# Optimization experiments

Hardware: AMD Instinct MI355X
Metric: run time of the kernel (lower is better)

## Reference

```python
import jax, jax.numpy as jnp
import numpy as np

DIM = 768
HEADS = 12
N_PATCH = 1024
ORDER = 5
DECAY = 0.5
EPS = 1e-6


def _exact_mask(N, order, decay):
    # 2D grid graph adjacency, row-major node order (matches sorted nx.grid_2d_graph nodes)
    side = int(np.sqrt(N))
    A = np.zeros((N, N), dtype=np.float64)
    idx = np.arange(N)
    r, c = idx // side, idx % side
    right = idx[c < side - 1]
    A[right, right + 1] = 1.0
    A[right + 1, right] = 1.0
    down = idx[r < side - 1]
    A[down, down + side] = 1.0
    A[down + side, down] = 1.0
    D_inv = 1.0 / np.maximum(A.sum(axis=1), 1.0)
    W = D_inv[:, None] * A
    M = np.eye(N)
    W_k = np.eye(N)
    coeff = 1.0
    for _ in range(order):
        W_k = W_k @ W
        coeff *= decay
        M += coeff * W_k
    M = M / M.sum(axis=1, keepdims=True)
    return jnp.asarray(M, dtype=jnp.float32)


def setup_inputs() -> dict:
    key = jax.random.key(0)
    k1, k2, k3, k4 = jax.random.split(key, 4)
    B = 4
    x = jax.random.normal(k1, (B, N_PATCH, DIM), dtype=jnp.float32)
    # nn.Linear(dim, 3*dim, bias=False): store as [dim, 3*dim] for x @ W
    scale = 1.0 / np.sqrt(DIM)
    W_qkv = jax.random.uniform(k2, (DIM, 3 * DIM), dtype=jnp.float32, minval=-scale, maxval=scale)
    W_out = jax.random.uniform(k3, (DIM, DIM), dtype=jnp.float32, minval=-scale, maxval=scale)
    b_out = jax.random.uniform(k4, (DIM,), dtype=jnp.float32, minval=-scale, maxval=scale)
    mask = _exact_mask(N_PATCH, ORDER, DECAY)
    return {"x": x, "W_qkv": W_qkv, "W_out": W_out, "b_out": b_out, "mask": mask}


def reference(x, W_qkv, W_out, b_out, mask):
    B, N, C = x.shape
    H, D = HEADS, C // HEADS
    qkv = x @ W_qkv  # [B, N, 3C]
    q, k, v = jnp.split(qkv, 3, axis=-1)
    # [B, N, C] -> [B, H, N, D]
    q, k, v = (t.reshape(B, N, H, D).transpose(0, 2, 1, 3) for t in (q, k, v))
    # feature map
    q = jax.nn.relu(q) + EPS
    k = jax.nn.relu(k) + EPS
    # (q^T @ M)^T = M^T @ q  ->  einsum over node axis
    q_graph = jnp.einsum('nm,bhnd->bhmd', mask, q)
    k_graph = jnp.einsum('nm,bhnd->bhmd', mask, k)
    q = q + 0.1 * q_graph
    k = k + 0.1 * k_graph
    linear_kernel = jnp.einsum('bhnd,bhmd->bhnm', q, k)  # [B, H, N, N]
    masked_kernel = linear_kernel * mask[None, None, :, :]
    z = 1.0 / (masked_kernel.sum(axis=-1, keepdims=True) + EPS)  # [B, H, N, 1]
    out = jnp.einsum('bhnm,bhmd->bhnd', masked_kernel, v) * z
    out = out.transpose(0, 2, 1, 3).reshape(B, N, C)
    return out @ W_out + b_out
```

## Files before the change

### kernel.cpp

```cpp
#include <hip/hip_runtime.h>

#define NP   1024
#define DIM  768
#define NH   12
#define HD   64
#define TQ   2304
#define EPS  1e-6f

typedef __attribute__((ext_vector_type(8))) short bf16x8;
typedef __attribute__((ext_vector_type(4))) float f32x4;

#define MFMA(a, b, c) __builtin_amdgcn_mfma_f32_16x16x32_bf16((a), (b), (c), 0, 0, 0)

__device__ __forceinline__ unsigned short f2b(float x) {
    unsigned int u = __builtin_bit_cast(unsigned int, x);
    u = (u + 0x7fffu + ((u >> 16) & 1u)) >> 16;
    return (unsigned short)u;
}
__device__ __forceinline__ float b2f(unsigned short h) {
    unsigned int u = ((unsigned int)h) << 16;
    return __builtin_bit_cast(float, u);
}
#if __has_builtin(__builtin_amdgcn_cvt_pk_bf16_f32)
typedef __attribute__((ext_vector_type(2))) __bf16 bf16x2t;
__device__ __forceinline__ unsigned int pk2(float lo, float hi) {
    bf16x2t v = __builtin_amdgcn_cvt_pk_bf16_f32(lo, hi);
    return __builtin_bit_cast(unsigned int, v);
}
#else
__device__ __forceinline__ unsigned int pk2(float lo, float hi) {
    return (unsigned int)f2b(lo) | ((unsigned int)f2b(hi) << 16);
}
#endif
__device__ __forceinline__ void gld16(const void* g, void* l) {
    __builtin_amdgcn_global_load_lds((const __attribute__((address_space(1))) unsigned int*)g,
                                     (__attribute__((address_space(3))) unsigned int*)l,
                                     16, 0, 0);
}

__global__ __launch_bounds__(256) void k_prep(const float* __restrict__ x,
                                              const float* __restrict__ W_qkv,
                                              const float* __restrict__ W_out,
                                              const float* __restrict__ mask,
                                              unsigned short* __restrict__ xb,
                                              unsigned short* __restrict__ WqkvT,
                                              unsigned short* __restrict__ WoutT,
                                              unsigned short* __restrict__ M2) {
    __shared__ float buf[64][65];
    const int bx = blockIdx.x, t = threadIdx.x;
    if (bx < 1536) {
        const int i = bx * 256 + t;
        const float4* p = (const float4*)x + (size_t)i * 2;
        float4 a = p[0], b = p[1];
        alignas(16) unsigned short o[8] = {f2b(a.x), f2b(a.y), f2b(a.z), f2b(a.w),
                                           f2b(b.x), f2b(b.y), f2b(b.z), f2b(b.w)};
        *(uint4*)(xb + (size_t)i * 8) = *(const uint4*)o;
        return;
    }
    const float* in; unsigned short* outp; int R, C, ct, rt; bool isMask = false;
    if (bx < 1968)      { int q = bx - 1536; in = W_qkv; outp = WqkvT; R = 768;  C = 2304; ct = q % 36; rt = q / 36; }
    else if (bx < 2112) { int q = bx - 1968; in = W_out; outp = WoutT; R = 768;  C = 768;  ct = q % 12; rt = q / 12; }
    else                { int q = bx - 2112; in = mask;  outp = M2;    R = 1024; C = 1024; ct = q % 16; rt = q / 16; isMask = true; }
    const int r0 = rt * 64, c0 = ct * 64;
    const int rr = t >> 4, cc = (t & 15) * 4;
    #pragma unroll
    for (int p = 0; p < 4; ++p) {
        float4 v = *(const float4*)(in + (size_t)(r0 + p * 16 + rr) * C + c0 + cc);
        buf[p * 16 + rr][cc + 0] = v.x; buf[p * 16 + rr][cc + 1] = v.y;
        buf[p * 16 + rr][cc + 2] = v.z; buf[p * 16 + rr][cc + 3] = v.w;
    }
    __syncthreads();
    const int oc = t >> 2, orr = (t & 3) * 16;
    alignas(16) unsigned short tmp[16];
    if (isMask) {
        #pragma unroll
        for (int j = 0; j < 16; ++j) {
            float v = 0.1f * buf[orr + j][oc] + ((c0 + oc) == (r0 + orr + j) ? 1.f : 0.f);
            tmp[j] = f2b(v);
        }
    } else {
        #pragma unroll
        for (int j = 0; j < 16; ++j) tmp[j] = f2b(buf[orr + j][oc]);
    }
    unsigned short* dst = outp + (size_t)(c0 + oc) * R + r0 + orr;
    *(uint4*)dst = *(const uint4*)tmp;
    *(uint4*)(dst + 8) = *(const uint4*)(tmp + 8);
}

__global__ __launch_bounds__(512) void k_gemm1(const unsigned short* __restrict__ A,
                                               const unsigned short* __restrict__ Bt,
                                               unsigned short* __restrict__ T) {
    __shared__ unsigned short As[128][32];
    __shared__ unsigned short Bs[128][32];
    const int tid = threadIdx.x, w = tid >> 6, l = tid & 63;
    const int bid = blockIdx.x;
    const int mstrip = (bid & 7) * 4 + ((bid >> 3) & 3);
    const int nstrip = bid >> 5;
    const int m0 = mstrip * 128, n0 = nstrip * 128;
    const int wm = (w & 3) * 32, wn = (w >> 2) * 64;
    const int quad = l >> 4, col = l & 15;
    const int lr = l >> 2, lc = (l & 3) * 8;

    f32x4 acc[2][4] = {};
    for (int k0 = 0; k0 < DIM; k0 += 32) {
        gld16(A + (size_t)(m0 + w * 16 + lr) * DIM + k0 + lc, &As[w * 16][0]);
        gld16(Bt + (size_t)(n0 + w * 16 + lr) * DIM + k0 + lc, &Bs[w * 16][0]);
        __syncthreads();
        bf16x8 a[2], b[4];
        #pragma unroll
        for (int i = 0; i < 2; ++i) a[i] = *(const bf16x8*)&As[wm + i * 16 + col][quad * 8];
        #pragma unroll
        for (int j = 0; j < 4; ++j) b[j] = *(const bf16x8*)&Bs[wn + j * 16 + col][quad * 8];
        #pragma unroll
        for (int i = 0; i < 2; ++i)
            #pragma unroll
            for (int j = 0; j < 4; ++j)
                acc[i][j] = MFMA(a[i], b[j], acc[i][j]);
        __syncthreads();
    }

    const int cgb = n0 + wn;
    const int slot = cgb / DIM;
    const int h = (cgb % DIM) >> 6;
    const bool act = (slot < 2);
    const int sh = slot * 48 + (m0 >> 10) * NH + h;
    const int npb = (m0 & 1023) + wm + quad * 4;
    #pragma unroll
    for (int j = 0; j < 4; ++j) {
        unsigned short* dcol = T + ((size_t)(sh * HD + j * 16 + col)) * NP + npb;
        #pragma unroll
        for (int i = 0; i < 2; ++i) {
            float v0 = acc[i][j][0], v1 = acc[i][j][1], v2 = acc[i][j][2], v3 = acc[i][j][3];
            if (act) {
                v0 = fmaxf(v0, 0.f) + EPS; v1 = fmaxf(v1, 0.f) + EPS;
                v2 = fmaxf(v2, 0.f) + EPS; v3 = fmaxf(v3, 0.f) + EPS;
            }
            uint2 o; o.x = pk2(v0, v1); o.y = pk2(v2, v3);
            *(uint2*)(dcol + i * 16) = o;
        }
    }
}

__global__ __launch_bounds__(256) void k_graphmix(const unsigned short* __restrict__ M2,
                                                  const unsigned short* __restrict__ T,
                                                  unsigned short* __restrict__ q2) {
    const int bh = blockIdx.y, mt = blockIdx.x;
    const int m0 = mt * 64;
    __shared__ unsigned short M2s[2][64][32], Fq[2][64][32], Fk[2][64][32];
    const int tid = threadIdx.x, w = tid >> 6, l = tid & 63;
    const int quad = l >> 4, col = l & 15;
    const int lr = l >> 2, lc = (l & 3) * 8;
    const unsigned short* Tq = T + (size_t)bh * HD * NP;
    const unsigned short* Tk = T + (size_t)(48 + bh) * HD * NP;

    f32x4 accq[4] = {}, acck[4] = {};
    const int c0 = max(0, mt - 3), c1 = min(15, mt + 3);
    for (int c = c0; c <= c1; ++c) {
        const int nc = c * 64;
        __syncthreads();
        #pragma unroll
        for (int hh = 0; hh < 2; ++hh) {
            gld16(M2 + (size_t)(m0 + w * 16 + lr) * NP + nc + hh * 32 + lc, &M2s[hh][w * 16][0]);
            gld16(Tq + (size_t)(w * 16 + lr) * NP + nc + hh * 32 + lc, &Fq[hh][w * 16][0]);
            gld16(Tk + (size_t)(w * 16 + lr) * NP + nc + hh * 32 + lc, &Fk[hh][w * 16][0]);
        }
        __syncthreads();
        #pragma unroll
        for (int ks = 0; ks < 2; ++ks) {
            bf16x8 bm = *(const bf16x8*)&M2s[ks][w * 16 + col][quad * 8];
            #pragma unroll
            for (int dt = 0; dt < 4; ++dt) {
                bf16x8 aq = *(const bf16x8*)&Fq[ks][dt * 16 + col][quad * 8];
                bf16x8 ak = *(const bf16x8*)&Fk[ks][dt * 16 + col][quad * 8];
                accq[dt] = MFMA(aq, bm, accq[dt]);
                acck[dt] = MFMA(ak, bm, acck[dt]);
            }
        }
    }
    unsigned short* q2q = q2 + ((size_t)bh * NP + m0 + w * 16 + col) * HD;
    unsigned short* q2k = q2 + ((size_t)(48 + bh) * NP + m0 + w * 16 + col) * HD;
    #pragma unroll
    for (int dt = 0; dt < 4; ++dt) {
        const int d0 = dt * 16 + quad * 4;
        uint2 oq; oq.x = pk2(accq[dt][0], accq[dt][1]); oq.y = pk2(accq[dt][2], accq[dt][3]);
        uint2 ok; ok.x = pk2(acck[dt][0], acck[dt][1]); ok.y = pk2(acck[dt][2], acck[dt][3]);
        *(uint2*)(q2q + d0) = oq;
        *(uint2*)(q2k + d0) = ok;
    }
}

__global__ __launch_bounds__(256) void k_attn(const unsigned short* __restrict__ q2,
                                              const unsigned short* __restrict__ T,
                                              const float* __restrict__ mask,
                                              unsigned short* __restrict__ attnb) {
    const int bh = blockIdx.y, b = bh / NH, h = bh % NH;
    const int nt = blockIdx.x, n0 = nt * 64;
    __shared__ unsigned short Qs[2][64][32];
    __shared__ unsigned short Ks[2][64][32];
    __shared__ unsigned short VT[2][64][32];
    __shared__ unsigned int Ss2[32][68];
    __shared__ float rowz[64];
    const int tid = threadIdx.x, w = tid >> 6, l = tid & 63;
    const int quad = l >> 4, col = l & 15;
    const int lr = l >> 2, lc = (l & 3) * 8;

    const unsigned short* qb = q2 + ((size_t)bh * NP + n0) * HD;
    const unsigned short* kb = q2 + (size_t)(48 + bh) * NP * HD;
    const unsigned short* vtb = T + (size_t)(96 + bh) * HD * NP;

    #pragma unroll
    for (int hh = 0; hh < 2; ++hh)
        gld16(qb + (size_t)(w * 16 + lr) * HD + hh * 32 + lc, &Qs[hh][w * 16][0]);

    f32x4 oacc[4] = {};
    float racc[4] = {};
    const int mlo = max(0, nt - 3), mhi = min(15, nt + 3);
    const unsigned int sel = (col & 1) ? 0x07060302u : 0x05040100u;

    for (int mt = mlo; mt <= mhi; ++mt) {
        const int m0 = mt * 64;
        __syncthreads();
        #pragma unroll
        for (int hh = 0; hh < 2; ++hh) {
            gld16(kb + (size_t)(m0 + w * 16 + lr) * HD + hh * 32 + lc, &Ks[hh][w * 16][0]);
            gld16(vtb + (size_t)(w * 16 + lr) * NP + m0 + hh * 32 + lc, &VT[hh][w * 16][0]);
        }
        float mreg[4][4];
        #pragma unroll
        for (int mtt = 0; mtt < 4; ++mtt)
            #pragma unroll
            for (int r = 0; r < 4; ++r)
                mreg[mtt][r] = mask[(size_t)(n0 + w * 16 + quad * 4 + r) * NP
                                    + m0 + mtt * 16 + col];
        __syncthreads();

        f32x4 s[4] = {};
        #pragma unroll
        for (int ks = 0; ks < 2; ++ks) {
            bf16x8 aq = *(const bf16x8*)&Qs[ks][w * 16 + col][quad * 8];
            #pragma unroll
            for (int mtt = 0; mtt < 4; ++mtt) {
                bf16x8 bk = *(const bf16x8*)&Ks[ks][mtt * 16 + col][quad * 8];
                s[mtt] = MFMA(aq, bk, s[mtt]);
            }
        }
        {
            const int npr = w * 8 + quad * 2;
            #pragma unroll
            for (int mtt = 0; mtt < 4; ++mtt) {
                float v0 = s[mtt][0] * mreg[mtt][0];
                float v1 = s[mtt][1] * mreg[mtt][1];
                float v2 = s[mtt][2] * mreg[mtt][2];
                float v3 = s[mtt][3] * mreg[mtt][3];
                racc[0] += v0; racc[1] += v1; racc[2] += v2; racc[3] += v3;
                Ss2[npr][mtt * 16 + col]     = pk2(v0, v1);
                Ss2[npr + 1][mtt * 16 + col] = pk2(v2, v3);
            }
        }
        __syncthreads();
        #pragma unroll
        for (int ks = 0; ks < 2; ++ks) {
            const unsigned int* rp = &Ss2[w * 8 + (col >> 1)][ks * 32 + quad * 8];
            uint4 U  = *(const uint4*)rp;
            uint4 U2 = *(const uint4*)(rp + 4);
            uint4 fr;
            fr.x = __builtin_amdgcn_perm(U.y,  U.x,  sel);
            fr.y = __builtin_amdgcn_perm(U.w,  U.z,  sel);
            fr.z = __builtin_amdgcn_perm(U2.y, U2.x, sel);
            fr.w = __builtin_amdgcn_perm(U2.w, U2.z, sel);
            bf16x8 as = __builtin_bit_cast(bf16x8, fr);
            #pragma unroll
            for (int dt = 0; dt < 4; ++dt) {
                bf16x8 bv = *(const bf16x8*)&VT[ks][dt * 16 + col][quad * 8];
                oacc[dt] = MFMA(as, bv, oacc[dt]);
            }
        }
    }

    #pragma unroll
    for (int r = 0; r < 4; ++r) {
        float v = racc[r];
        v += __shfl_xor(v, 1); v += __shfl_xor(v, 2);
        v += __shfl_xor(v, 4); v += __shfl_xor(v, 8);
        if (col == 0) rowz[w * 16 + quad * 4 + r] = v;
    }
    __syncthreads();
    #pragma unroll
    for (int r = 0; r < 4; ++r) {
        const int nl = w * 16 + quad * 4 + r;
        const float z = 1.f / (rowz[nl] + EPS);
        #pragma unroll
        for (int dt = 0; dt < 4; ++dt)
            attnb[(size_t)(b * NP + n0 + nl) * DIM + h * HD + dt * 16 + col] =
                f2b(oacc[dt][r] * z);
    }
}

__global__ __launch_bounds__(256) void k_gemm2(const unsigned short* __restrict__ A,
                                               const unsigned short* __restrict__ Bt,
                                               const float* __restrict__ bias,
                                               float* __restrict__ C) {
    __shared__ unsigned short As[128][32];
    __shared__ unsigned short Bs[64][32];
    const int tid = threadIdx.x, w = tid >> 6, l = tid & 63;
    const int bid = blockIdx.x;
    const int mstrip = (bid & 7) * 4 + ((bid >> 3) & 3);
    const int nstrip = bid >> 5;
    const int m0 = mstrip * 128, n0 = nstrip * 64;
    const int wm = (w >> 1) * 64, wn = (w & 1) * 32;
    const int quad = l >> 4, col = l & 15;
    const int lr = l >> 2, lc = (l & 3) * 8;

    f32x4 acc[4][2] = {};
    for (int k0 = 0; k0 < DIM; k0 += 32) {
        gld16(A + (size_t)(m0 + w * 32 + lr) * DIM + k0 + lc, &As[w * 32][0]);
        gld16(A + (size_t)(m0 + w * 32 + 16 + lr) * DIM + k0 + lc, &As[w * 32 + 16][0]);
        gld16(Bt + (size_t)(n0 + w * 16 + lr) * DIM + k0 + lc, &Bs[w * 16][0]);
        __syncthreads();
        bf16x8 a[4], b[2];
        #pragma unroll
        for (int i = 0; i < 4; ++i) a[i] = *(const bf16x8*)&As[wm + i * 16 + col][quad * 8];
        #pragma unroll
        for (int j = 0; j < 2; ++j) b[j] = *(const bf16x8*)&Bs[wn + j * 16 + col][quad * 8];
        #pragma unroll
        for (int i = 0; i < 4; ++i)
            #pragma unroll
            for (int j = 0; j < 2; ++j)
                acc[i][j] = MFMA(a[i], b[j], acc[i][j]);
        __syncthreads();
    }
    #pragma unroll
    for (int i = 0; i < 4; ++i)
        #pragma unroll
        for (int j = 0; j < 2; ++j) {
            const int n = n0 + wn + j * 16 + col;
            #pragma unroll
            for (int r = 0; r < 4; ++r) {
                const int m = m0 + wm + i * 16 + quad * 4 + r;
                C[(size_t)m * DIM + n] = acc[i][j][r] + bias[n];
            }
        }
}

extern "C" void kernel_launch(void* const* d_in, const int* in_sizes, int n_in,
                              void* d_out, int out_size, void* d_ws, size_t ws_size,
                              hipStream_t stream) {
    (void)in_sizes; (void)n_in; (void)out_size; (void)ws_size;
    const float* x     = (const float*)d_in[0];
    const float* W_qkv = (const float*)d_in[1];
    const float* W_out = (const float*)d_in[2];
    const float* b_out = (const float*)d_in[3];
    const float* mask  = (const float*)d_in[4];
    float* out = (float*)d_out;

    unsigned short* p = (unsigned short*)d_ws;
    unsigned short* xb    = p; p += (size_t)4096 * DIM;
    unsigned short* WqkvT = p; p += (size_t)TQ * DIM;
    unsigned short* WoutT = p; p += (size_t)DIM * DIM;
    unsigned short* M2    = p; p += (size_t)NP * NP;
    unsigned short* T     = p; p += (size_t)3 * 48 * HD * NP;
    unsigned short* q2    = p; p += (size_t)2 * 48 * NP * HD;
    unsigned short* attnb = p; p += (size_t)4096 * DIM;

    k_prep<<<dim3(2368), 256, 0, stream>>>(x, W_qkv, W_out, mask, xb, WqkvT, WoutT, M2);
    k_gemm1<<<dim3(576), 512, 0, stream>>>(xb, WqkvT, T);
    k_graphmix<<<dim3(NP / 64, 48), 256, 0, stream>>>(M2, T, q2);
    k_attn<<<dim3(NP / 64, 48), 256, 0, stream>>>(q2, T, mask, attnb);
    k_gemm2<<<dim3(384), 256, 0, stream>>>(attnb, WoutT, b_out, out);
}
```

Before: 163.0 us.

## Fuse x bf16 conversion into QKV GEMM, tighten band windows, retile output GEMM

The separate x-to-bf16 pass in the prep kernel is removed; the QKV GEMM now reads fp32 x directly and converts it while staging into LDS, which saves a full write and re-read of the activation. The QKV and output GEMMs now process 64-wide K steps (two 32-wide halves per sync), halving barrier count. The graph-mix and attention band loops switch from seven 64-wide tiles to a 32-aligned window of 384 columns, trimming work outside the mask band. The output GEMM uses 64x64 tiles with twice as many blocks to improve occupancy, at the cost of more redundant operand loads.

New measurement: 156.8 us. 3.8% less time.

```diff
diff --git a/kernel.cpp b/kernel.cpp
--- a/kernel.cpp
+++ b/kernel.cpp
@@ -38,29 +38,18 @@
                                      16, 0, 0);
 }
 
-__global__ __launch_bounds__(256) void k_prep(const float* __restrict__ x,
-                                              const float* __restrict__ W_qkv,
+__global__ __launch_bounds__(256) void k_prep(const float* __restrict__ W_qkv,
                                               const float* __restrict__ W_out,
                                               const float* __restrict__ mask,
-                                              unsigned short* __restrict__ xb,
                                               unsigned short* __restrict__ WqkvT,
                                               unsigned short* __restrict__ WoutT,
                                               unsigned short* __restrict__ M2) {
     __shared__ float buf[64][65];
     const int bx = blockIdx.x, t = threadIdx.x;
-    if (bx < 1536) {
-        const int i = bx * 256 + t;
-        const float4* p = (const float4*)x + (size_t)i * 2;
-        float4 a = p[0], b = p[1];
-        alignas(16) unsigned short o[8] = {f2b(a.x), f2b(a.y), f2b(a.z), f2b(a.w),
-                                           f2b(b.x), f2b(b.y), f2b(b.z), f2b(b.w)};
-        *(uint4*)(xb + (size_t)i * 8) = *(const uint4*)o;
-        return;
-    }
     const float* in; unsigned short* outp; int R, C, ct, rt; bool isMask = false;
-    if (bx < 1968)      { int q = bx - 1536; in = W_qkv; outp = WqkvT; R = 768;  C = 2304; ct = q % 36; rt = q / 36; }
-    else if (bx < 2112) { int q = bx - 1968; in = W_out; outp = WoutT; R = 768;  C = 768;  ct = q % 12; rt = q / 12; }
-    else                { int q = bx - 2112; in = mask;  outp = M2;    R = 1024; C = 1024; ct = q % 16; rt = q / 16; isMask = true; }
+    if (bx < 432)      { int q = bx;       in = W_qkv; outp = WqkvT; R = 768;  C = 2304; ct = q % 36; rt = q / 36; }
+    else if (bx < 576) { int q = bx - 432; in = W_out; outp = WoutT; R = 768;  C = 768;  ct = q % 12; rt = q / 12; }
+    else               { int q = bx - 576; in = mask;  outp = M2;    R = 1024; C = 1024; ct = q % 16; rt = q / 16; isMask = true; }
     const int r0 = rt * 64, c0 = ct * 64;
     const int rr = t >> 4, cc = (t & 15) * 4;
     #pragma unroll
@@ -87,11 +76,11 @@
     *(uint4*)(dst + 8) = *(const uint4*)(tmp + 8);
 }
 
-__global__ __launch_bounds__(512) void k_gemm1(const unsigned short* __restrict__ A,
+__global__ __launch_bounds__(512) void k_gemm1(const float* __restrict__ X,
                                                const unsigned short* __restrict__ Bt,
                                                unsigned short* __restrict__ T) {
-    __shared__ unsigned short As[128][32];
-    __shared__ unsigned short Bs[128][32];
+    __shared__ unsigned short As[2][128][32];
+    __shared__ unsigned short Bs[2][128][32];
     const int tid = threadIdx.x, w = tid >> 6, l = tid & 63;
     const int bid = blockIdx.x;
     const int mstrip = (bid & 7) * 4 + ((bid >> 3) & 3);
@@ -100,22 +89,35 @@
     const int wm = (w & 3) * 32, wn = (w >> 2) * 64;
     const int quad = l >> 4, col = l & 15;
     const int lr = l >> 2, lc = (l & 3) * 8;
+    const int arow = tid >> 2, akc = (tid & 3) * 8;
 
     f32x4 acc[2][4] = {};
-    for (int k0 = 0; k0 < DIM; k0 += 32) {
-        gld16(A + (size_t)(m0 + w * 16 + lr) * DIM + k0 + lc, &As[w * 16][0]);
-        gld16(Bt + (size_t)(n0 + w * 16 + lr) * DIM + k0 + lc, &Bs[w * 16][0]);
-        __syncthreads();
-        bf16x8 a[2], b[4];
-        #pragma unroll
-        for (int i = 0; i < 2; ++i) a[i] = *(const bf16x8*)&As[wm + i * 16 + col][quad * 8];
-        #pragma unroll
-        for (int j = 0; j < 4; ++j) b[j] = *(const bf16x8*)&Bs[wn + j * 16 + col][quad * 8];
-        #pragma unroll
-        for (int i = 0; i < 2; ++i)
-            #pragma unroll
-            for (int j = 0; j < 4; ++j)
-                acc[i][j] = MFMA(a[i], b[j], acc[i][j]);
+    for (int k0 = 0; k0 < DIM; k0 += 64) {
+        #pragma unroll
+        for (int hh = 0; hh < 2; ++hh) {
+            gld16(Bt + (size_t)(n0 + w * 16 + lr) * DIM + k0 + hh * 32 + lc, &Bs[hh][w * 16][0]);
+            const float* xp = X + (size_t)(m0 + arow) * DIM + k0 + hh * 32 + akc;
+            float4 xa = *(const float4*)xp;
+            float4 xb = *(const float4*)(xp + 4);
+            uint4 o;
+            o.x = pk2(xa.x, xa.y); o.y = pk2(xa.z, xa.w);
+            o.z = pk2(xb.x, xb.y); o.w = pk2(xb.z, xb.w);
+            *(uint4*)&As[hh][arow][akc] = o;
+        }
+        __syncthreads();
+        #pragma unroll
+        for (int hh = 0; hh < 2; ++hh) {
+            bf16x8 a[2], b[4];
+            #pragma unroll
+            for (int i = 0; i < 2; ++i) a[i] = *(const bf16x8*)&As[hh][wm + i * 16 + col][quad * 8];
+            #pragma unroll
+            for (int j = 0; j < 4; ++j) b[j] = *(const bf16x8*)&Bs[hh][wn + j * 16 + col][quad * 8];
+            #pragma unroll
+            for (int i = 0; i < 2; ++i)
+                #pragma unroll
+                for (int j = 0; j < 4; ++j)
+                    acc[i][j] = MFMA(a[i], b[j], acc[i][j]);
+        }
         __syncthreads();
     }
 
@@ -146,7 +148,7 @@
                                                   unsigned short* __restrict__ q2) {
     const int bh = blockIdx.y, mt = blockIdx.x;
     const int m0 = mt * 64;
-    __shared__ unsigned short M2s[2][64][32], Fq[2][64][32], Fk[2][64][32];
+    __shared__ unsigned short M2s[4][64][32], Fq[4][64][32], Fk[4][64][32];
     const int tid = threadIdx.x, w = tid >> 6, l = tid & 63;
     const int quad = l >> 4, col = l & 15;
     const int lr = l >> 2, lc = (l & 3) * 8;
@@ -154,19 +156,19 @@
     const unsigned short* Tk = T + (size_t)(48 + bh) * HD * NP;
 
     f32x4 accq[4] = {}, acck[4] = {};
-    const int c0 = max(0, mt - 3), c1 = min(15, mt + 3);
-    for (int c = c0; c <= c1; ++c) {
-        const int nc = c * 64;
-        __syncthreads();
-        #pragma unroll
-        for (int hh = 0; hh < 2; ++hh) {
+    const int nr0 = min(max(2 * mt - 5, 0), 20) * 32;
+    for (int it = 0; it < 3; ++it) {
+        const int nc = nr0 + it * 128;
+        __syncthreads();
+        #pragma unroll
+        for (int hh = 0; hh < 4; ++hh) {
             gld16(M2 + (size_t)(m0 + w * 16 + lr) * NP + nc + hh * 32 + lc, &M2s[hh][w * 16][0]);
             gld16(Tq + (size_t)(w * 16 + lr) * NP + nc + hh * 32 + lc, &Fq[hh][w * 16][0]);
             gld16(Tk + (size_t)(w * 16 + lr) * NP + nc + hh * 32 + lc, &Fk[hh][w * 16][0]);
         }
         __syncthreads();
         #pragma unroll
-        for (int ks = 0; ks < 2; ++ks) {
+        for (int ks = 0; ks < 4; ++ks) {
             bf16x8 bm = *(const bf16x8*)&M2s[ks][w * 16 + col][quad * 8];
             #pragma unroll
             for (int dt = 0; dt < 4; ++dt) {
@@ -214,11 +216,11 @@
 
     f32x4 oacc[4] = {};
     float racc[4] = {};
-    const int mlo = max(0, nt - 3), mhi = min(15, nt + 3);
+    const int mr0 = min(max(2 * nt - 5, 0), 20) * 32;
     const unsigned int sel = (col & 1) ? 0x07060302u : 0x05040100u;
 
-    for (int mt = mlo; mt <= mhi; ++mt) {
-        const int m0 = mt * 64;
+    for (int it = 0; it < 6; ++it) {
+        const int m0 = mr0 + it * 64;
         __syncthreads();
         #pragma unroll
         for (int hh = 0; hh < 2; ++hh) {
@@ -300,37 +302,42 @@
                                                const unsigned short* __restrict__ Bt,
                                                const float* __restrict__ bias,
                                                float* __restrict__ C) {
-    __shared__ unsigned short As[128][32];
-    __shared__ unsigned short Bs[64][32];
+    __shared__ unsigned short As[2][64][32];
+    __shared__ unsigned short Bs[2][64][32];
     const int tid = threadIdx.x, w = tid >> 6, l = tid & 63;
     const int bid = blockIdx.x;
-    const int mstrip = (bid & 7) * 4 + ((bid >> 3) & 3);
-    const int nstrip = bid >> 5;
-    const int m0 = mstrip * 128, n0 = nstrip * 64;
-    const int wm = (w >> 1) * 64, wn = (w & 1) * 32;
+    const int mstrip = (bid & 7) * 8 + ((bid >> 3) & 7);
+    const int nstrip = bid >> 6;
+    const int m0 = mstrip * 64, n0 = nstrip * 64;
+    const int wm = (w & 1) * 32, wn = (w >> 1) * 32;
     const int quad = l >> 4, col = l & 15;
     const int lr = l >> 2, lc = (l & 3) * 8;
 
-    f32x4 acc[4][2] = {};
-    for (int k0 = 0; k0 < DIM; k0 += 32) {
-        gld16(A + (size_t)(m0 + w * 32 + lr) * DIM + k0 + lc, &As[w * 32][0]);
-        gld16(A + (size_t)(m0 + w * 32 + 16 + lr) * DIM + k0 + lc, &As[w * 32 + 16][0]);
-        gld16(Bt + (size_t)(n0 + w * 16 + lr) * DIM + k0 + lc, &Bs[w * 16][0]);
-        __syncthreads();
-        bf16x8 a[4], b[2];
-        #pragma unroll
-        for (int i = 0; i < 4; ++i) a[i] = *(const bf16x8*)&As[wm + i * 16 + col][quad * 8];
-        #pragma unroll
-        for (int j = 0; j < 2; ++j) b[j] = *(const bf16x8*)&Bs[wn + j * 16 + col][quad * 8];
-        #pragma unroll
-        for (int i = 0; i < 4; ++i)
-            #pragma unroll
-            for (int j = 0; j < 2; ++j)
-                acc[i][j] = MFMA(a[i], b[j], acc[i][j]);
-        __syncthreads();
-    }
-    #pragma unroll
-    for (int i = 0; i < 4; ++i)
+    f32x4 acc[2][2] = {};
+    for (int k0 = 0; k0 < DIM; k0 += 64) {
+        #pragma unroll
+        for (int hh = 0; hh < 2; ++hh) {
+            gld16(A + (size_t)(m0 + w * 16 + lr) * DIM + k0 + hh * 32 + lc, &As[hh][w * 16][0]);
+            gld16(Bt + (size_t)(n0 + w * 16 + lr) * DIM + k0 + hh * 32 + lc, &Bs[hh][w * 16][0]);
+        }
+        __syncthreads();
+        #pragma unroll
+        for (int hh = 0; hh < 2; ++hh) {
+            bf16x8 a[2], b[2];
+            #pragma unroll
+            for (int i = 0; i < 2; ++i) a[i] = *(const bf16x8*)&As[hh][wm + i * 16 + col][quad * 8];
+            #pragma unroll
+            for (int j = 0; j < 2; ++j) b[j] = *(const bf16x8*)&Bs[hh][wn + j * 16 + col][quad * 8];
+            #pragma unroll
+            for (int i = 0; i < 2; ++i)
+                #pragma unroll
+                for (int j = 0; j < 2; ++j)
+                    acc[i][j] = MFMA(a[i], b[j], acc[i][j]);
+        }
+        __syncthreads();
+    }
+    #pragma unroll
+    for (int i = 0; i < 2; ++i)
         #pragma unroll
         for (int j = 0; j < 2; ++j) {
             const int n = n0 + wn + j * 16 + col;
@@ -354,7 +361,6 @@
     float* out = (float*)d_out;
 
     unsigned short* p = (unsigned short*)d_ws;
-    unsigned short* xb    = p; p += (size_t)4096 * DIM;
     unsigned short* WqkvT = p; p += (size_t)TQ * DIM;
     unsigned short* WoutT = p; p += (size_t)DIM * DIM;
     unsigned short* M2    = p; p += (size_t)NP * NP;
@@ -362,9 +368,9 @@
     unsigned short* q2    = p; p += (size_t)2 * 48 * NP * HD;
     unsigned short* attnb = p; p += (size_t)4096 * DIM;
 
-    k_prep<<<dim3(2368), 256, 0, stream>>>(x, W_qkv, W_out, mask, xb, WqkvT, WoutT, M2);
-    k_gemm1<<<dim3(576), 512, 0, stream>>>(xb, WqkvT, T);
+    k_prep<<<dim3(832), 256, 0, stream>>>(W_qkv, W_out, mask, WqkvT, WoutT, M2);
+    k_gemm1<<<dim3(576), 512, 0, stream>>>(x, WqkvT, T);
     k_graphmix<<<dim3(NP / 64, 48), 256, 0, stream>>>(M2, T, q2);
     k_attn<<<dim3(NP / 64, 48), 256, 0, stream>>>(q2, T, mask, attnb);
-    k_gemm2<<<dim3(384), 256, 0, stream>>>(attnb, WoutT, b_out, out);
-}
+    k_gemm2<<<dim3(768), 256, 0, stream>>>(attnb, WoutT, b_out, out);
+}
```
